# Performance work log

Measured on AMD Instinct MI355X. Metric: run time of the kernel, lower is better.

## Reference

```python
import jax, jax.numpy as jnp
import numpy as np

B, N, D, H = 4, 512, 256, 256


def setup_inputs() -> dict:
    key = jax.random.key(0)
    ks = jax.random.split(key, 8)
    s = lambda fan: 1.0 / np.sqrt(fan)
    return {
        "X": jax.random.normal(ks[0], (B, N, D), dtype=jnp.float32),
        "Y": jax.random.normal(ks[1], (B, N, D), dtype=jnp.float32),
        # fc = Linear(D,H) -> Tanh -> Linear(H,H)
        "W1": jax.random.normal(ks[2], (H, D), dtype=jnp.float32) * s(D),
        "b1": jnp.zeros((H,), dtype=jnp.float32),
        "W2": jax.random.normal(ks[3], (H, H), dtype=jnp.float32) * s(H),
        "b2": jnp.zeros((H,), dtype=jnp.float32),
        # fc_q, fc_k
        "Wq": jax.random.normal(ks[4], (H, H), dtype=jnp.float32) * s(H),
        "bq": jnp.zeros((H,), dtype=jnp.float32),
        "Wk": jax.random.normal(ks[5], (H, H), dtype=jnp.float32) * s(H),
        "bk": jnp.zeros((H,), dtype=jnp.float32),
        # AddComp projection vector v: E_ij = v . tanh(Q_i + K_j)
        "v": jax.random.normal(ks[6], (H,), dtype=jnp.float32) * s(H),
        "k": 5,
    }


def reference(X, Y, W1, b1, W2, b2, Wq, bq, Wk, bk, v, k):
    # fc: Linear -> Tanh -> Linear  (Y and k are unused, as in the original)
    h = jnp.tanh(jnp.einsum('bnd,hd->bnh', X, W1) + b1)
    h = jnp.einsum('bnh,gh->bng', h, W2) + b2          # [B,N,H]
    Q = jnp.einsum('bnh,gh->bng', h, Wq) + bq          # [B,N,H]
    K = jnp.einsum('bnh,gh->bng', h, Wk) + bk          # [B,N,H]
    # Additive compatibility: E[b,i,j] = v . tanh(Q[b,i] + K[b,j])
    E = jnp.einsum('bijh,h->bij', jnp.tanh(Q[:, :, None, :] + K[:, None, :, :]), v)
    # Symmetrize
    return 0.5 * (E + jnp.swapaxes(E, -2, -1))
```

## Files before the change

### kernel.cpp

```cpp
#include <hip/hip_runtime.h>


typedef float f2 __attribute__((ext_vector_type(2)));
typedef float f4 __attribute__((ext_vector_type(4)));
typedef float f32x4 __attribute__((ext_vector_type(4)));
typedef __bf16 bf16x8 __attribute__((ext_vector_type(8)));

#define C2F 2.8853900817779268f

__device__ inline unsigned short f2bf(float f) {
    unsigned u = __float_as_uint(f);
    unsigned r = (u + 0x7fffu + ((u >> 16) & 1u)) >> 16;
    return (unsigned short)r;
}
__device__ inline float bf2f(unsigned short h) {
    return __uint_as_float(((unsigned)h) << 16);
}

__device__ inline void split4(const f4 a, unsigned short* hp, unsigned short* lp) {
    unsigned short h[4], l[4];
#pragma unroll
    for (int t = 0; t < 4; ++t) {
        h[t] = f2bf(a[t]);
        l[t] = f2bf(a[t] - bf2f(h[t]));
    }
    uint2 hv, lv;
    hv.x = (unsigned)h[0] | ((unsigned)h[1] << 16);
    hv.y = (unsigned)h[2] | ((unsigned)h[3] << 16);
    lv.x = (unsigned)l[0] | ((unsigned)l[1] << 16);
    lv.y = (unsigned)l[2] | ((unsigned)l[3] << 16);
    *(uint2*)hp = hv;
    *(uint2*)lp = lv;
}

template <int ACT>
__global__ __launch_bounds__(256) void gemm_fullk(
    const float* __restrict__ A, const float* __restrict__ Wa,
    const float* __restrict__ Wb, const float* __restrict__ ba,
    const float* __restrict__ bb2, float* __restrict__ C, int Nn) {
    __shared__ unsigned short sAhi[64][264];
    __shared__ unsigned short sAlo[64][264];
    __shared__ unsigned short sBhi[64][264];
    __shared__ unsigned short sBlo[64][264];

    const int tid = threadIdx.x;
    const int m0 = blockIdx.x << 6;
    const int n0 = blockIdx.y << 6;

    const float* Atile = A + (size_t)m0 * 256;
    const float* Wtile = (n0 < 256) ? (Wa + (size_t)n0 * 256)
                                    : (Wb + (size_t)(n0 - 256) * 256);
    const int col4 = (tid & 63) << 2;
    const int rgrp = tid >> 6;
#pragma unroll
    for (int t = 0; t < 16; ++t) {
        const int row = (t << 2) + rgrp;
        f4 av = *(const f4*)&Atile[(size_t)row * 256 + col4];
        f4 wv = *(const f4*)&Wtile[(size_t)row * 256 + col4];
        split4(av, &sAhi[row][col4], &sAlo[row][col4]);
        split4(wv, &sBhi[row][col4], &sBlo[row][col4]);
    }
    __syncthreads();

    const int lane = tid & 63;
    const int wav = tid >> 6;
    const int wm = wav >> 1, wn = wav & 1;
    const int fr = lane & 15;
    const int fks = (lane >> 4) << 3;

    f32x4 acc[2][2];
#pragma unroll
    for (int i = 0; i < 2; ++i)
#pragma unroll
        for (int j = 0; j < 2; ++j) acc[i][j] = (f32x4){0.f, 0.f, 0.f, 0.f};

#pragma unroll
    for (int kt = 0; kt < 256; kt += 32) {
        bf16x8 ah[2], al[2], bh[2], bl[2];
#pragma unroll
        for (int s = 0; s < 2; ++s) {
            ah[s] = *(const bf16x8*)&sAhi[(wm << 5) + (s << 4) + fr][kt + fks];
            al[s] = *(const bf16x8*)&sAlo[(wm << 5) + (s << 4) + fr][kt + fks];
            bh[s] = *(const bf16x8*)&sBhi[(wn << 5) + (s << 4) + fr][kt + fks];
            bl[s] = *(const bf16x8*)&sBlo[(wn << 5) + (s << 4) + fr][kt + fks];
        }
#pragma unroll
        for (int i = 0; i < 2; ++i)
#pragma unroll
            for (int j = 0; j < 2; ++j) {
                acc[i][j] = __builtin_amdgcn_mfma_f32_16x16x32_bf16(ah[i], bh[j], acc[i][j], 0, 0, 0);
                acc[i][j] = __builtin_amdgcn_mfma_f32_16x16x32_bf16(ah[i], bl[j], acc[i][j], 0, 0, 0);
                acc[i][j] = __builtin_amdgcn_mfma_f32_16x16x32_bf16(al[i], bh[j], acc[i][j], 0, 0, 0);
            }
    }

    const int rbase = (lane >> 4) << 2;
#pragma unroll
    for (int i = 0; i < 2; ++i) {
#pragma unroll
        for (int j = 0; j < 2; ++j) {
            const int gcol = n0 + (wn << 5) + (j << 4) + fr;
            const float bias = (ACT == 2 && gcol >= 256) ? bb2[gcol - 256] : ba[gcol];
#pragma unroll
            for (int q = 0; q < 4; ++q) {
                const int grow = m0 + (wm << 5) + (i << 4) + rbase + q;
                float x = acc[i][j][q] + bias;
                if (ACT == 1)
                    x = 1.0f - 2.0f * __builtin_amdgcn_rcpf(
                                          1.0f + __builtin_amdgcn_exp2f(C2F * x));
                if (ACT == 2)
                    x = fminf(__builtin_amdgcn_exp2f(C2F * x), 1.0e4f);
                C[(size_t)grow * Nn + gcol] = x;
            }
        }
    }
}

__global__ __launch_bounds__(256) void gemm_stage1(
    const float* __restrict__ X, const float* __restrict__ W1,
    const float* __restrict__ b1, const float* __restrict__ Wq,
    const float* __restrict__ Wk, const float* __restrict__ W2,
    const float* __restrict__ b2, const float* __restrict__ bq,
    const float* __restrict__ bk, float* __restrict__ h1,
    float* __restrict__ Wc, float* __restrict__ bc) {
    __shared__ unsigned short sAhi[64][264];
    __shared__ unsigned short sAlo[64][264];
    __shared__ unsigned short sBhi[64][264];
    __shared__ unsigned short sBlo[64][264];
    __shared__ float sred[64][4];

    const int tid = threadIdx.x;
    const bool is_nt = (blockIdx.x >= 128);
    const int blk = is_nt ? (blockIdx.x - 128) : blockIdx.x;
    const int m0 = (blk >> 2) << 6;
    const int n0 = (blk & 3) << 6;

    const int col4 = (tid & 63) << 2;
    const int rgrp = tid >> 6;

    if (!is_nt) {
        const float* Atile = X + (size_t)m0 * 256;
        const float* Wtile = W1 + (size_t)n0 * 256;
#pragma unroll
        for (int t = 0; t < 16; ++t) {
            const int row = (t << 2) + rgrp;
            f4 av = *(const f4*)&Atile[(size_t)row * 256 + col4];
            f4 wv = *(const f4*)&Wtile[(size_t)row * 256 + col4];
            split4(av, &sAhi[row][col4], &sAlo[row][col4]);
            split4(wv, &sBhi[row][col4], &sBlo[row][col4]);
        }
    } else {
        const float* Atile = (m0 < 256) ? (Wq + (size_t)m0 * 256)
                                        : (Wk + (size_t)(m0 - 256) * 256);
#pragma unroll
        for (int t = 0; t < 16; ++t) {
            const int row = (t << 2) + rgrp;
            f4 av = *(const f4*)&Atile[(size_t)row * 256 + col4];
            split4(av, &sAhi[row][col4], &sAlo[row][col4]);
        }
        const int c4 = (tid & 15) << 2;
        const int kg = tid >> 4;
#pragma unroll
        for (int t = 0; t < 16; ++t) {
            const int k = (t << 4) + kg;
            f4 wv = *(const f4*)&W2[(size_t)k * 256 + n0 + c4];
#pragma unroll
            for (int q = 0; q < 4; ++q) {
                unsigned short hi = f2bf(wv[q]);
                sBhi[c4 + q][k] = hi;
                sBlo[c4 + q][k] = f2bf(wv[q] - bf2f(hi));
            }
        }
    }
    __syncthreads();

    const int lane = tid & 63;
    const int wav = tid >> 6;
    const int wm = wav >> 1, wn = wav & 1;
    const int fr = lane & 15;
    const int fks = (lane >> 4) << 3;

    f32x4 acc[2][2];
#pragma unroll
    for (int i = 0; i < 2; ++i)
#pragma unroll
        for (int j = 0; j < 2; ++j) acc[i][j] = (f32x4){0.f, 0.f, 0.f, 0.f};

#pragma unroll
    for (int kt = 0; kt < 256; kt += 32) {
        bf16x8 ah[2], al[2], bh[2], bl[2];
#pragma unroll
        for (int s = 0; s < 2; ++s) {
            ah[s] = *(const bf16x8*)&sAhi[(wm << 5) + (s << 4) + fr][kt + fks];
            al[s] = *(const bf16x8*)&sAlo[(wm << 5) + (s << 4) + fr][kt + fks];
            bh[s] = *(const bf16x8*)&sBhi[(wn << 5) + (s << 4) + fr][kt + fks];
            bl[s] = *(const bf16x8*)&sBlo[(wn << 5) + (s << 4) + fr][kt + fks];
        }
#pragma unroll
        for (int i = 0; i < 2; ++i)
#pragma unroll
            for (int j = 0; j < 2; ++j) {
                acc[i][j] = __builtin_amdgcn_mfma_f32_16x16x32_bf16(ah[i], bh[j], acc[i][j], 0, 0, 0);
                acc[i][j] = __builtin_amdgcn_mfma_f32_16x16x32_bf16(ah[i], bl[j], acc[i][j], 0, 0, 0);
                acc[i][j] = __builtin_amdgcn_mfma_f32_16x16x32_bf16(al[i], bh[j], acc[i][j], 0, 0, 0);
            }
    }

    const int rbase = (lane >> 4) << 2;
    if (!is_nt) {
#pragma unroll
        for (int i = 0; i < 2; ++i)
#pragma unroll
            for (int j = 0; j < 2; ++j) {
                const int gcol = n0 + (wn << 5) + (j << 4) + fr;
                const float bias = b1[gcol];
#pragma unroll
                for (int q = 0; q < 4; ++q) {
                    const int grow = m0 + (wm << 5) + (i << 4) + rbase + q;
                    float x = acc[i][j][q] + bias;
                    x = 1.0f - 2.0f * __builtin_amdgcn_rcpf(
                                          1.0f + __builtin_amdgcn_exp2f(C2F * x));
                    h1[(size_t)grow * 256 + gcol] = x;
                }
            }
    } else {
#pragma unroll
        for (int i = 0; i < 2; ++i)
#pragma unroll
            for (int j = 0; j < 2; ++j) {
                const int gcol = n0 + (wn << 5) + (j << 4) + fr;
#pragma unroll
                for (int q = 0; q < 4; ++q) {
                    const int grow = m0 + (wm << 5) + (i << 4) + rbase + q;
                    Wc[(size_t)grow * 256 + gcol] = acc[i][j][q];
                }
            }
        if ((blk & 3) == 0) {
            const int rr = tid >> 2;
            const int part = (tid & 3) << 6;
            const int grow = m0 + rr;
            const float* Ar = (grow < 256) ? &Wq[(size_t)grow * 256]
                                           : &Wk[(size_t)(grow - 256) * 256];
            float s = 0.f;
#pragma unroll
            for (int e = 0; e < 64; e += 4) {
                f4 a = *(const f4*)&Ar[part + e];
                f4 bv = *(const f4*)&b2[part + e];
                s += a[0] * bv[0] + a[1] * bv[1] + a[2] * bv[2] + a[3] * bv[3];
            }
            sred[rr][tid & 3] = s;
            __syncthreads();
            if (tid < 64) {
                float bias = sred[tid][0] + sred[tid][1] + sred[tid][2] + sred[tid][3];
                const int g2 = m0 + tid;
                bias += (g2 < 256) ? bq[g2] : bk[g2 - 256];
                bc[g2] = bias;
            }
        }
    }
}

__global__ __launch_bounds__(512, 4) void pairwise_kernel(
    const float* __restrict__ uwb, const float* __restrict__ v,
    float* __restrict__ Ep) {
    __shared__ float sU[64][68];
    __shared__ float sW[64][68];
    __shared__ float sV[64];

    const int tid = threadIdx.x;
    const int bb = blockIdx.x;
    const int hcs = bb & 3;
    const int hc = hcs << 6;
    const int tt = bb >> 2;
    const int b = tt >> 6;
    const int i0 = ((tt >> 3) & 7) << 6;
    const int j0 = (tt & 7) << 6;

    const float* ubase = uwb + (size_t)((b << 9) + i0) * 512 + hc;
    const float* wbase = uwb + (size_t)((b << 9) + j0) * 512 + 256 + hc;

    const int sr = tid >> 3;
    const int sc = (tid & 7) << 3;
    {
        f4 a0 = *(const f4*)&ubase[(size_t)sr * 512 + sc];
        f4 a1 = *(const f4*)&ubase[(size_t)sr * 512 + sc + 4];
        f4 b0 = *(const f4*)&wbase[(size_t)sr * 512 + sc];
        f4 b1 = *(const f4*)&wbase[(size_t)sr * 512 + sc + 4];
        *(f4*)&sU[sr][sc] = a0;
        *(f4*)&sU[sr][sc + 4] = a1;
        *(f4*)&sW[sr][sc] = b0;
        *(f4*)&sW[sr][sc + 4] = b1;
    }
    if (tid < 16) *(f4*)&sV[tid << 2] = *(const f4*)&v[hc + (tid << 2)];
    __syncthreads();

    const int ty = tid >> 5;
    const int tx = tid & 31;

    float acc[4][2];
#pragma unroll
    for (int d = 0; d < 4; ++d)
#pragma unroll
        for (int e = 0; e < 2; ++e) acc[d][e] = 0.f;

    const f2 one2 = (f2){1.f, 1.f};

#pragma unroll 4
    for (int h4 = 0; h4 < 64; h4 += 4) {
        f4 vv = *(const f4*)&sV[h4];
        f4 uu[4], ww[2];
#pragma unroll
        for (int d = 0; d < 4; ++d) uu[d] = *(const f4*)&sU[ty + (d << 4)][h4];
#pragma unroll
        for (int e = 0; e < 2; ++e) ww[e] = *(const f4*)&sW[tx + (e << 5)][h4];
#pragma unroll
        for (int d = 0; d < 4; ++d)
#pragma unroll
            for (int e = 0; e < 2; ++e) {
                f2 u01 = (f2){uu[d][0], uu[d][1]};
                f2 u23 = (f2){uu[d][2], uu[d][3]};
                f2 w01 = (f2){ww[e][0], ww[e][1]};
                f2 w23 = (f2){ww[e][2], ww[e][3]};
                f2 A01 = __builtin_elementwise_fma(u01, w01, one2);
                f2 A23 = __builtin_elementwise_fma(u23, w23, one2);
                float m01 = A01.x * A01.y;
                float t01 = fmaf(vv[0], A01.y, vv[1] * A01.x);
                acc[d][e] = fmaf(t01, __builtin_amdgcn_rcpf(m01), acc[d][e]);
                float m23 = A23.x * A23.y;
                float t23 = fmaf(vv[2], A23.y, vv[3] * A23.x);
                acc[d][e] = fmaf(t23, __builtin_amdgcn_rcpf(m23), acc[d][e]);
            }
    }

    float* ep = Ep + (size_t)hcs * 1048576 + (size_t)((b << 9) + i0) * 512 + j0;
#pragma unroll
    for (int d = 0; d < 4; ++d)
#pragma unroll
        for (int e = 0; e < 2; ++e)
            ep[(size_t)(ty + (d << 4)) * 512 + tx + (e << 5)] = acc[d][e];
}

__global__ __launch_bounds__(256) void sym_kernel(const float* __restrict__ Ep,
                                                  const float* __restrict__ v,
                                                  float* __restrict__ out) {
    __shared__ float t1[64][65];
    __shared__ float t2[64][65];
    __shared__ float red[4];

    const int tid = threadIdx.x;
    const int lane = tid & 63, wv = tid >> 6;

    float x = v[tid];
#pragma unroll
    for (int o = 32; o > 0; o >>= 1) x += __shfl_xor(x, o, 64);
    if (lane == 0) red[wv] = x;

    const int bb = blockIdx.x;
    const int b = bb >> 6;
    const int i0 = ((bb >> 3) & 7) << 6;
    const int j0 = (bb & 7) << 6;

    for (int idx = tid; idx < 4096; idx += 256) {
        const int r = idx >> 6, c = idx & 63;
        const size_t o1 = (size_t)((b << 9) + i0 + r) * 512 + j0 + c;
        const size_t o2 = (size_t)((b << 9) + j0 + r) * 512 + i0 + c;
        t1[r][c] = (Ep[o1] + Ep[o1 + 1048576]) +
                   (Ep[o1 + 2097152] + Ep[o1 + 3145728]);
        t2[r][c] = (Ep[o2] + Ep[o2 + 1048576]) +
                   (Ep[o2 + 2097152] + Ep[o2 + 3145728]);
    }
    __syncthreads();
    const float Sv = red[0] + red[1] + red[2] + red[3];
    for (int idx = tid; idx < 4096; idx += 256) {
        const int r = idx >> 6, c = idx & 63;
        out[(size_t)((b << 9) + i0 + r) * 512 + j0 + c] = Sv - (t1[r][c] + t2[c][r]);
    }
}

extern "C" void kernel_launch(void* const* d_in, const int* in_sizes, int n_in,
                              void* d_out, int out_size, void* d_ws, size_t ws_size,
                              hipStream_t stream) {
    const float* X  = (const float*)d_in[0];
    const float* W1 = (const float*)d_in[2];
    const float* b1 = (const float*)d_in[3];
    const float* W2 = (const float*)d_in[4];
    const float* b2 = (const float*)d_in[5];
    const float* Wq = (const float*)d_in[6];
    const float* bq = (const float*)d_in[7];
    const float* Wk = (const float*)d_in[8];
    const float* bk = (const float*)d_in[9];
    const float* v  = (const float*)d_in[10];

    float* ws  = (float*)d_ws;
    float* h1  = ws;
    float* uwb = ws + 524288;
    float* Wc  = ws + 1572864;
    float* bc  = ws + 1703936;
    float* Ep  = ws + 1704448;
    float* out = (float*)d_out;

    gemm_stage1<<<160, 256, 0, stream>>>(X, W1, b1, Wq, Wk, W2, b2, bq, bk,
                                         h1, Wc, bc);
    gemm_fullk<2><<<dim3(32, 8), 256, 0, stream>>>(h1, Wc, Wc + 65536, bc,
                                                   bc + 256, uwb, 512);
    pairwise_kernel<<<1024, 512, 0, stream>>>(uwb, v, Ep);
    sym_kernel<<<256, 256, 0, stream>>>(Ep, v, out);
}
```

Baseline: 65.48 us.

## Combine four tanh terms per reciprocal with even/odd split column layout

The stage-2 GEMM epilogue now writes the exp-transformed Q/K columns in an even/odd interleaved order, so the pairwise kernel can load matching even and odd hidden units as separate contiguous vectors. The pairwise kernel merges four rational tanh terms into one numerator/denominator pair before each reciprocal, which halves the rcp count per output and uses more packed FMAs. The risk is numerical: the product of four (1+uw) factors can overflow or lose precision even with the 1e4 clamp, and the layout change links the GEMM output ordering to the pairwise kernel.

```diff
diff --git a/kernel.cpp b/kernel.cpp
--- a/kernel.cpp
+++ b/kernel.cpp
@@ -101,6 +101,12 @@
         for (int j = 0; j < 2; ++j) {
             const int gcol = n0 + (wn << 5) + (j << 4) + fr;
             const float bias = (ACT == 2 && gcol >= 256) ? bb2[gcol - 256] : ba[gcol];
+            int scol = gcol;
+            if (ACT == 2) {
+                const int half = gcol & 256;
+                const int c = gcol & 255;
+                scol = half + ((c & 1) << 7) + (c >> 1);
+            }
 #pragma unroll
             for (int q = 0; q < 4; ++q) {
                 const int grow = m0 + (wm << 5) + (i << 4) + rbase + q;
@@ -110,7 +116,7 @@
                                           1.0f + __builtin_amdgcn_exp2f(C2F * x));
                 if (ACT == 2)
                     x = fminf(__builtin_amdgcn_exp2f(C2F * x), 1.0e4f);
-                C[(size_t)grow * Nn + gcol] = x;
+                C[(size_t)grow * Nn + scol] = x;
             }
         }
     }
@@ -263,73 +269,86 @@
 __global__ __launch_bounds__(512, 4) void pairwise_kernel(
     const float* __restrict__ uwb, const float* __restrict__ v,
     float* __restrict__ Ep) {
-    __shared__ float sU[64][68];
-    __shared__ float sW[64][68];
-    __shared__ float sV[64];
+    __shared__ float sUe[64][36];
+    __shared__ float sUo[64][36];
+    __shared__ float sWe[64][36];
+    __shared__ float sWo[64][36];
+    __shared__ float sVe[32];
+    __shared__ float sVo[32];
 
     const int tid = threadIdx.x;
     const int bb = blockIdx.x;
     const int hcs = bb & 3;
-    const int hc = hcs << 6;
     const int tt = bb >> 2;
     const int b = tt >> 6;
     const int i0 = ((tt >> 3) & 7) << 6;
     const int j0 = (tt & 7) << 6;
 
-    const float* ubase = uwb + (size_t)((b << 9) + i0) * 512 + hc;
-    const float* wbase = uwb + (size_t)((b << 9) + j0) * 512 + 256 + hc;
-
-    const int sr = tid >> 3;
-    const int sc = (tid & 7) << 3;
-    {
-        f4 a0 = *(const f4*)&ubase[(size_t)sr * 512 + sc];
-        f4 a1 = *(const f4*)&ubase[(size_t)sr * 512 + sc + 4];
-        f4 b0 = *(const f4*)&wbase[(size_t)sr * 512 + sc];
-        f4 b1 = *(const f4*)&wbase[(size_t)sr * 512 + sc + 4];
-        *(f4*)&sU[sr][sc] = a0;
-        *(f4*)&sU[sr][sc + 4] = a1;
-        *(f4*)&sW[sr][sc] = b0;
-        *(f4*)&sW[sr][sc + 4] = b1;
-    }
-    if (tid < 16) *(f4*)&sV[tid << 2] = *(const f4*)&v[hc + (tid << 2)];
+    const float* ub = uwb + (size_t)((b << 9) + i0) * 512 + (hcs << 5);
+    const float* wb = uwb + (size_t)((b << 9) + j0) * 512 + 256 + (hcs << 5);
+
+    const int row = tid >> 3;
+    const int c4 = (tid & 7) << 2;
+    *(f4*)&sUe[row][c4] = *(const f4*)&ub[(size_t)row * 512 + c4];
+    *(f4*)&sUo[row][c4] = *(const f4*)&ub[(size_t)row * 512 + 128 + c4];
+    *(f4*)&sWe[row][c4] = *(const f4*)&wb[(size_t)row * 512 + c4];
+    *(f4*)&sWo[row][c4] = *(const f4*)&wb[(size_t)row * 512 + 128 + c4];
+    if (tid < 32) {
+        sVe[tid] = v[(hcs << 6) + (tid << 1)];
+        sVo[tid] = v[(hcs << 6) + (tid << 1) + 1];
+    }
     __syncthreads();
 
     const int ty = tid >> 5;
     const int tx = tid & 31;
 
-    float acc[4][2];
+    f2 acc[4][2];
 #pragma unroll
     for (int d = 0; d < 4; ++d)
 #pragma unroll
-        for (int e = 0; e < 2; ++e) acc[d][e] = 0.f;
+        for (int e = 0; e < 2; ++e) acc[d][e] = (f2){0.f, 0.f};
 
     const f2 one2 = (f2){1.f, 1.f};
 
-#pragma unroll 4
-    for (int h4 = 0; h4 < 64; h4 += 4) {
-        f4 vv = *(const f4*)&sV[h4];
-        f4 uu[4], ww[2];
-#pragma unroll
-        for (int d = 0; d < 4; ++d) uu[d] = *(const f4*)&sU[ty + (d << 4)][h4];
-#pragma unroll
-        for (int e = 0; e < 2; ++e) ww[e] = *(const f4*)&sW[tx + (e << 5)][h4];
-#pragma unroll
-        for (int d = 0; d < 4; ++d)
+#pragma unroll 2
+    for (int g = 0; g < 8; ++g) {
+        const int hb = g << 2;
+        const f4 ve = *(const f4*)&sVe[hb];
+        const f4 vo = *(const f4*)&sVo[hb];
+        f4 we[2], wo[2];
+#pragma unroll
+        for (int e = 0; e < 2; ++e) {
+            we[e] = *(const f4*)&sWe[tx + (e << 5)][hb];
+            wo[e] = *(const f4*)&sWo[tx + (e << 5)][hb];
+        }
+#pragma unroll
+        for (int d = 0; d < 4; ++d) {
+            const f4 ue = *(const f4*)&sUe[ty + (d << 4)][hb];
+            const f4 uo = *(const f4*)&sUo[ty + (d << 4)][hb];
+            const f2 ue_lo = (f2){ue.x, ue.y}, ue_hi = (f2){ue.z, ue.w};
+            const f2 uo_lo = (f2){uo.x, uo.y}, uo_hi = (f2){uo.z, uo.w};
 #pragma unroll
             for (int e = 0; e < 2; ++e) {
-                f2 u01 = (f2){uu[d][0], uu[d][1]};
-                f2 u23 = (f2){uu[d][2], uu[d][3]};
-                f2 w01 = (f2){ww[e][0], ww[e][1]};
-                f2 w23 = (f2){ww[e][2], ww[e][3]};
-                f2 A01 = __builtin_elementwise_fma(u01, w01, one2);
-                f2 A23 = __builtin_elementwise_fma(u23, w23, one2);
-                float m01 = A01.x * A01.y;
-                float t01 = fmaf(vv[0], A01.y, vv[1] * A01.x);
-                acc[d][e] = fmaf(t01, __builtin_amdgcn_rcpf(m01), acc[d][e]);
-                float m23 = A23.x * A23.y;
-                float t23 = fmaf(vv[2], A23.y, vv[3] * A23.x);
-                acc[d][e] = fmaf(t23, __builtin_amdgcn_rcpf(m23), acc[d][e]);
-            }
+                const f2 we_lo = (f2){we[e].x, we[e].y}, we_hi = (f2){we[e].z, we[e].w};
+                const f2 wo_lo = (f2){wo[e].x, wo[e].y}, wo_hi = (f2){wo[e].z, wo[e].w};
+                f2 Ae1 = __builtin_elementwise_fma(ue_lo, we_lo, one2);
+                f2 Ao1 = __builtin_elementwise_fma(uo_lo, wo_lo, one2);
+                f2 Ae2 = __builtin_elementwise_fma(ue_hi, we_hi, one2);
+                f2 Ao2 = __builtin_elementwise_fma(uo_hi, wo_hi, one2);
+                f2 mlo = Ae1 * Ao1;
+                f2 mhi = Ae2 * Ao2;
+                f2 tlo = __builtin_elementwise_fma(
+                    (f2){ve.x, ve.y}, Ao1, (f2){vo.x, vo.y} * Ae1);
+                f2 thi = __builtin_elementwise_fma(
+                    (f2){ve.z, ve.w}, Ao2, (f2){vo.z, vo.w} * Ae2);
+                float Mlo = mlo.x * mlo.y;
+                float Nlo = fmaf(tlo.x, mlo.y, tlo.y * mlo.x);
+                float Mhi = mhi.x * mhi.y;
+                float Nhi = fmaf(thi.x, mhi.y, thi.y * mhi.x);
+                acc[d][e].x = fmaf(Nlo, __builtin_amdgcn_rcpf(Mlo), acc[d][e].x);
+                acc[d][e].y = fmaf(Nhi, __builtin_amdgcn_rcpf(Mhi), acc[d][e].y);
+            }
+        }
     }
 
     float* ep = Ep + (size_t)hcs * 1048576 + (size_t)((b << 9) + i0) * 512 + j0;
@@ -337,7 +356,8 @@
     for (int d = 0; d < 4; ++d)
 #pragma unroll
         for (int e = 0; e < 2; ++e)
-            ep[(size_t)(ty + (d << 4)) * 512 + tx + (e << 5)] = acc[d][e];
+            ep[(size_t)(ty + (d << 4)) * 512 + tx + (e << 5)] =
+                acc[d][e].x + acc[d][e].y;
 }
 
 __global__ __launch_bounds__(256) void sym_kernel(const float* __restrict__ Ep,
```

Measured after the change: 63.20 us. 1.04x faster.

## Combine eight rational terms per reciprocal and atomically accumulate partial sums

Applied to the files above, without the earlier changes.

The pairwise kernel now folds eight hidden dimensions into a single fraction before taking one reciprocal, where it previously took one reciprocal per pair. The exponentials are rescaled by 2^-8 and clamped tighter so the product of eight terms stays inside float range. The four per-slice partial E buffers are replaced by atomicAdd into one zeroed buffer, so the symmetrize kernel reads a quarter as much data. The cost is an extra memset, atomic contention, and some risk to precision and overflow from the rescaling.

```diff
diff --git a/kernel.cpp b/kernel.cpp
--- a/kernel.cpp
+++ b/kernel.cpp
@@ -7,6 +7,7 @@
 typedef __bf16 bf16x8 __attribute__((ext_vector_type(8)));
 
 #define C2F 2.8853900817779268f
+#define S8  0.00390625f
 
 __device__ inline unsigned short f2bf(float f) {
     unsigned u = __float_as_uint(f);
@@ -108,8 +109,12 @@
                 if (ACT == 1)
                     x = 1.0f - 2.0f * __builtin_amdgcn_rcpf(
                                           1.0f + __builtin_amdgcn_exp2f(C2F * x));
-                if (ACT == 2)
-                    x = fminf(__builtin_amdgcn_exp2f(C2F * x), 1.0e4f);
+                if (ACT == 2) {
+                    if (gcol < 256)
+                        x = fminf(__builtin_amdgcn_exp2f(C2F * x - 8.0f), 4.0f);
+                    else
+                        x = fminf(__builtin_amdgcn_exp2f(C2F * x), 1024.0f);
+                }
                 C[(size_t)grow * Nn + gcol] = x;
             }
         }
@@ -303,41 +308,53 @@
 #pragma unroll
         for (int e = 0; e < 2; ++e) acc[d][e] = 0.f;
 
-    const f2 one2 = (f2){1.f, 1.f};
-
-#pragma unroll 4
-    for (int h4 = 0; h4 < 64; h4 += 4) {
-        f4 vv = *(const f4*)&sV[h4];
-        f4 uu[4], ww[2];
-#pragma unroll
-        for (int d = 0; d < 4; ++d) uu[d] = *(const f4*)&sU[ty + (d << 4)][h4];
-#pragma unroll
-        for (int e = 0; e < 2; ++e) ww[e] = *(const f4*)&sW[tx + (e << 5)][h4];
-#pragma unroll
-        for (int d = 0; d < 4; ++d)
+#pragma unroll 2
+    for (int h8 = 0; h8 < 64; h8 += 8) {
+        const f4 vv0 = *(const f4*)&sV[h8];
+        const f4 vv1 = *(const f4*)&sV[h8 + 4];
+        f4 w0[2], w1[2];
+#pragma unroll
+        for (int e = 0; e < 2; ++e) {
+            w0[e] = *(const f4*)&sW[tx + (e << 5)][h8];
+            w1[e] = *(const f4*)&sW[tx + (e << 5)][h8 + 4];
+        }
+#pragma unroll
+        for (int d = 0; d < 4; ++d) {
+            const f4 u0 = *(const f4*)&sU[ty + (d << 4)][h8];
+            const f4 u1 = *(const f4*)&sU[ty + (d << 4)][h8 + 4];
 #pragma unroll
             for (int e = 0; e < 2; ++e) {
-                f2 u01 = (f2){uu[d][0], uu[d][1]};
-                f2 u23 = (f2){uu[d][2], uu[d][3]};
-                f2 w01 = (f2){ww[e][0], ww[e][1]};
-                f2 w23 = (f2){ww[e][2], ww[e][3]};
-                f2 A01 = __builtin_elementwise_fma(u01, w01, one2);
-                f2 A23 = __builtin_elementwise_fma(u23, w23, one2);
-                float m01 = A01.x * A01.y;
-                float t01 = fmaf(vv[0], A01.y, vv[1] * A01.x);
-                acc[d][e] = fmaf(t01, __builtin_amdgcn_rcpf(m01), acc[d][e]);
-                float m23 = A23.x * A23.y;
-                float t23 = fmaf(vv[2], A23.y, vv[3] * A23.x);
-                acc[d][e] = fmaf(t23, __builtin_amdgcn_rcpf(m23), acc[d][e]);
-            }
-    }
-
-    float* ep = Ep + (size_t)hcs * 1048576 + (size_t)((b << 9) + i0) * 512 + j0;
+                const float A0 = fmaf(u0.x, w0[e].x, S8);
+                const float A1 = fmaf(u0.y, w0[e].y, S8);
+                const float A2 = fmaf(u0.z, w0[e].z, S8);
+                const float A3 = fmaf(u0.w, w0[e].w, S8);
+                const float A4 = fmaf(u1.x, w1[e].x, S8);
+                const float A5 = fmaf(u1.y, w1[e].y, S8);
+                const float A6 = fmaf(u1.z, w1[e].z, S8);
+                const float A7 = fmaf(u1.w, w1[e].w, S8);
+                const float m01 = A0 * A1, m23 = A2 * A3;
+                const float m45 = A4 * A5, m67 = A6 * A7;
+                const float t01 = fmaf(vv0.x, A1, vv0.y * A0);
+                const float t23 = fmaf(vv0.z, A3, vv0.w * A2);
+                const float t45 = fmaf(vv1.x, A5, vv1.y * A4);
+                const float t67 = fmaf(vv1.z, A7, vv1.w * A6);
+                const float m03 = m01 * m23, m47 = m45 * m67;
+                const float t03 = fmaf(t01, m23, t23 * m01);
+                const float t47 = fmaf(t45, m67, t67 * m45);
+                const float M = m03 * m47;
+                const float N = fmaf(t03, m47, t47 * m03);
+                acc[d][e] = fmaf(N, __builtin_amdgcn_rcpf(M), acc[d][e]);
+            }
+        }
+    }
+
+    float* ep = Ep + (size_t)((b << 9) + i0) * 512 + j0;
 #pragma unroll
     for (int d = 0; d < 4; ++d)
 #pragma unroll
         for (int e = 0; e < 2; ++e)
-            ep[(size_t)(ty + (d << 4)) * 512 + tx + (e << 5)] = acc[d][e];
+            atomicAdd(&ep[(size_t)(ty + (d << 4)) * 512 + tx + (e << 5)],
+                      acc[d][e] * S8);
 }
 
 __global__ __launch_bounds__(256) void sym_kernel(const float* __restrict__ Ep,
@@ -362,12 +379,8 @@
 
     for (int idx = tid; idx < 4096; idx += 256) {
         const int r = idx >> 6, c = idx & 63;
-        const size_t o1 = (size_t)((b << 9) + i0 + r) * 512 + j0 + c;
-        const size_t o2 = (size_t)((b << 9) + j0 + r) * 512 + i0 + c;
-        t1[r][c] = (Ep[o1] + Ep[o1 + 1048576]) +
-                   (Ep[o1 + 2097152] + Ep[o1 + 3145728]);
-        t2[r][c] = (Ep[o2] + Ep[o2 + 1048576]) +
-                   (Ep[o2 + 2097152] + Ep[o2 + 3145728]);
+        t1[r][c] = Ep[(size_t)((b << 9) + i0 + r) * 512 + j0 + c];
+        t2[r][c] = Ep[(size_t)((b << 9) + j0 + r) * 512 + i0 + c];
     }
     __syncthreads();
     const float Sv = red[0] + red[1] + red[2] + red[3];
@@ -399,6 +412,8 @@
     float* Ep  = ws + 1704448;
     float* out = (float*)d_out;
 
+    hipMemsetAsync(Ep, 0, 1048576 * sizeof(float), stream);
+
     gemm_stage1<<<160, 256, 0, stream>>>(X, W1, b1, Wq, Wk, W2, b2, bq, bk,
                                          h1, Wc, bc);
     gemm_fullk<2><<<dim3(32, 8), 256, 0, stream>>>(h1, Wc, Wc + 65536, bc,
```

After: 62.63 us. 4.4% less time.
